# Performance work log

Measured on AMD Instinct MI355X. Metric: run time of the kernel, lower is better.

The kernel has to match this reference:

```python
import jax, jax.numpy as jnp
import numpy as np

N_NODES = 5000
N_EDGES = 80000
IN_DIM = 128
HID_DIM = 128
OUT_DIM = 64
NUM_HEADS = 1
BATCH = 8
NEG_SLOPE = 0.2  # DGL GATConv default leaky_relu negative_slope


def setup_inputs() -> dict:
    key = jax.random.key(0)
    ks = jax.random.split(key, 12)
    x = jax.random.normal(ks[0], (BATCH, N_NODES, IN_DIM), dtype=jnp.float32)
    src = jax.random.randint(ks[1], (N_EDGES,), 0, N_NODES)
    dst = jax.random.randint(ks[2], (N_EDGES,), 0, N_NODES)
    # layer1 params (fc has no bias in DGL GATConv; output bias present by default)
    s1 = 1.0 / np.sqrt(IN_DIM)
    W1 = jax.random.normal(ks[3], (IN_DIM, NUM_HEADS * HID_DIM), dtype=jnp.float32) * s1
    al1 = jax.random.normal(ks[4], (NUM_HEADS, HID_DIM), dtype=jnp.float32) * 0.1
    ar1 = jax.random.normal(ks[5], (NUM_HEADS, HID_DIM), dtype=jnp.float32) * 0.1
    b1 = jnp.zeros((NUM_HEADS * HID_DIM,), dtype=jnp.float32)
    # layer2 params
    s2 = 1.0 / np.sqrt(NUM_HEADS * HID_DIM)
    W2 = jax.random.normal(ks[6], (NUM_HEADS * HID_DIM, NUM_HEADS * OUT_DIM), dtype=jnp.float32) * s2
    al2 = jax.random.normal(ks[7], (NUM_HEADS, OUT_DIM), dtype=jnp.float32) * 0.1
    ar2 = jax.random.normal(ks[8], (NUM_HEADS, OUT_DIM), dtype=jnp.float32) * 0.1
    b2 = jnp.zeros((NUM_HEADS * OUT_DIM,), dtype=jnp.float32)
    return {"x": x, "W1": W1, "al1": al1, "ar1": ar1, "b1": b1,
            "W2": W2, "al2": al2, "ar2": ar2, "b2": b2,
            "src": src, "dst": dst}


def gat_layer(x, W, al, ar, b, src, dst, n_nodes):
    """DGL GATConv. x:[B,N,Din] W:[Din,H*F] al/ar:[H,F] b:[H*F] -> [B,N,H,F]."""
    B = x.shape[0]
    H, F = al.shape
    z = (x @ W).reshape(B, n_nodes, H, F)                 # [B,N,H,F]
    el = jnp.einsum('bnhf,hf->bnh', z, al)                # src-side attn term
    er = jnp.einsum('bnhf,hf->bnh', z, ar)                # dst-side attn term
    e = jax.nn.leaky_relu(el[:, src] + er[:, dst], NEG_SLOPE)  # [B,E,H]
    e = jnp.moveaxis(e, 1, 0)                             # [E,B,H]  edge-major for segment ops
    emax = jax.ops.segment_max(e, dst, num_segments=n_nodes)   # [N,B,H]
    ex = jnp.exp(e - emax[dst])
    denom = jax.ops.segment_sum(ex, dst, num_segments=n_nodes)  # [N,B,H]
    alpha = ex / denom[dst]                               # edge softmax over incoming edges
    zs = jnp.moveaxis(z[:, src], 1, 0)                    # [E,B,H,F] gathered source feats
    out = jax.ops.segment_sum(alpha[..., None] * zs, dst, num_segments=n_nodes)  # [N,B,H,F]
    return jnp.moveaxis(out, 0, 1) + b.reshape(1, 1, H, F)


def reference(x, W1, al1, ar1, b1, W2, al2, ar2, b2, src, dst):
    n_nodes = x.shape[1]
    h = gat_layer(x, W1, al1, ar1, b1, src, dst, n_nodes)  # [B,N,H,hid]
    B, N, H, Fh = h.shape
    h = h.reshape(B, N, H * Fh)                            # concat heads (H=1)
    o = gat_layer(h, W2, al2, ar2, b2, src, dst, n_nodes)  # [B,N,H,out]
    o = o.reshape(B * N, -1)                               # squeeze: [B*N, out]
    return jax.nn.softmax(o, axis=-1)
```

## Files before the change

kernel.cpp:

```cpp
#include <hip/hip_runtime.h>
#include <hip/hip_bf16.h>

#define N_NODES 5000
#define N_EDGES 80000
#define HID_DIM 128
#define OUT_DIM 64
#define BATCH 8
#define M_ROWS 40000
#define NEG_SLOPE 0.2f
#define BUCKET 96


typedef unsigned short ushort_t;
typedef unsigned int uint_t;
typedef __attribute__((ext_vector_type(8))) short short8;
typedef __attribute__((ext_vector_type(4))) float f32x4;

__device__ __forceinline__ float bf16_to_f32(ushort_t u) {
  return __uint_as_float(((uint_t)u) << 16);
}
__device__ __forceinline__ ushort_t f32_to_bf16(float f) {
  uint_t u = __float_as_uint(f);
  return (ushort_t)((u + 0x7FFF + ((u >> 16) & 1)) >> 16);
}

struct __attribute__((aligned(8))) us4 { ushort_t x, y, z, w; };

__global__ __launch_bounds__(256) void zero_pack_kernel(const float* __restrict__ W1,
                                                        const float* __restrict__ W2,
                                                        int* __restrict__ cnt,
                                                        ushort_t* __restrict__ Bp1,
                                                        ushort_t* __restrict__ Bp2) {
  int bid = blockIdx.x;
  if (bid < 20) {
    int i = bid * 256 + threadIdx.x;
    if (i < N_NODES) cnt[i] = 0;
    return;
  }
  int gid = (bid - 20) * 256 + threadIdx.x;
  if (gid >= 3072) return;
  const float* W; ushort_t* Bp; int NC, idx;
  if (gid < 2048) { W = W1; Bp = Bp1; NC = 128; idx = gid; }
  else            { W = W2; Bp = Bp2; NC = 64;  idx = gid - 2048; }
  int l = idx & 63, tt = idx >> 6;
  int T = NC / 16;
  int kc = tt / T, t = tt % T;
  int col = t * 16 + (l & 15);
  int krow = kc * 32 + (l >> 4) * 8;
  short8 vv;
#pragma unroll
  for (int j = 0; j < 8; j++) vv[j] = (short)f32_to_bf16(W[(size_t)(krow + j) * NC + col]);
  *(short8*)(Bp + (size_t)idx * 8) = vv;
}

template <int NC, bool A_F32, bool C_BF16, bool SCATTER>
__global__ __launch_bounds__(256) void gemm_mfma(const void* __restrict__ A,
                                                 const ushort_t* __restrict__ Bp,
                                                 void* __restrict__ C,
                                                 const float* __restrict__ al,
                                                 const float* __restrict__ ar,
                                                 float* __restrict__ el,
                                                 float* __restrict__ er,
                                                 const int* __restrict__ e_src,
                                                 const int* __restrict__ e_dst,
                                                 int* __restrict__ cnt,
                                                 int* __restrict__ srcs) {
  if (SCATTER) {
    int tid = threadIdx.x;
    if (tid < 128) {
      int i = blockIdx.x * 128 + tid;
      int d = e_dst[i];
      int pos = atomicAdd(&cnt[d], 1);
      if (pos < BUCKET) srcs[d * BUCKET + pos] = e_src[i];
    }
  }
  constexpr int T = NC / 16;
  int wave = threadIdx.x >> 6, lane = threadIdx.x & 63;
  int q = lane >> 4, m = lane & 15;
  int r0 = blockIdx.x * 64 + wave * 16;
  f32x4 acc[T];
#pragma unroll
  for (int t = 0; t < T; t++)
#pragma unroll
    for (int i = 0; i < 4; i++) acc[t][i] = 0.f;

  const short8* Bp8 = (const short8*)Bp;
  size_t arow = (size_t)(r0 + m) * 128;
#pragma unroll
  for (int kc = 0; kc < 4; kc++) {
    short8 af;
    if (A_F32) {
      const float* Ap = (const float*)A + arow + kc * 32 + q * 8;
      float4 v0 = *(const float4*)Ap;
      float4 v1 = *(const float4*)(Ap + 4);
      af[0] = (short)f32_to_bf16(v0.x); af[1] = (short)f32_to_bf16(v0.y);
      af[2] = (short)f32_to_bf16(v0.z); af[3] = (short)f32_to_bf16(v0.w);
      af[4] = (short)f32_to_bf16(v1.x); af[5] = (short)f32_to_bf16(v1.y);
      af[6] = (short)f32_to_bf16(v1.z); af[7] = (short)f32_to_bf16(v1.w);
    } else {
      const ushort_t* Ap = (const ushort_t*)A + arow + kc * 32 + q * 8;
      us4 a0 = *(const us4*)Ap;
      us4 a1 = *(const us4*)(Ap + 4);
      af[0] = (short)a0.x; af[1] = (short)a0.y; af[2] = (short)a0.z; af[3] = (short)a0.w;
      af[4] = (short)a1.x; af[5] = (short)a1.y; af[6] = (short)a1.z; af[7] = (short)a1.w;
    }
#pragma unroll
    for (int t = 0; t < T; t++) {
      short8 bf = Bp8[(kc * T + t) * 64 + lane];
      acc[t] = __builtin_amdgcn_mfma_f32_16x16x32_bf16(af, bf, acc[t], 0, 0, 0);
    }
  }
  float sl[4] = {0.f, 0.f, 0.f, 0.f}, sr[4] = {0.f, 0.f, 0.f, 0.f};
#pragma unroll
  for (int t = 0; t < T; t++) {
    float alv = al[t * 16 + m];
    float arv = ar[t * 16 + m];
#pragma unroll
    for (int i = 0; i < 4; i++) { sl[i] += acc[t][i] * alv; sr[i] += acc[t][i] * arv; }
  }
#pragma unroll
  for (int o = 1; o < 16; o <<= 1) {
#pragma unroll
    for (int i = 0; i < 4; i++) {
      sl[i] += __shfl_xor(sl[i], o, 64);
      sr[i] += __shfl_xor(sr[i], o, 64);
    }
  }
  if (m == 0) {
#pragma unroll
    for (int i = 0; i < 4; i++) {
      el[r0 + q * 4 + i] = sl[i];
      er[r0 + q * 4 + i] = sr[i];
    }
  }
#pragma unroll
  for (int t = 0; t < T; t++)
#pragma unroll
    for (int i = 0; i < 4; i++) {
      size_t off = (size_t)(r0 + q * 4 + i) * NC + t * 16 + m;
      if (C_BF16) ((ushort_t*)C)[off] = f32_to_bf16(acc[t][i]);
      else        ((float*)C)[off] = acc[t][i];
    }
}

template <int F, bool FINAL>
__global__ __launch_bounds__(256) void agg_kernel(const void* __restrict__ z,
                                                  const float* __restrict__ el,
                                                  const float* __restrict__ er,
                                                  const float* __restrict__ bias,
                                                  const int* __restrict__ cnt,
                                                  const int* __restrict__ srcs,
                                                  void* __restrict__ outp) {
  int id = (threadIdx.x >> 6) * gridDim.x + blockIdx.x;
  int lane = threadIdx.x & 63;
  int g = lane >> 4, l16 = lane & 15;
  int b = id & 7, n = id >> 3;
  int deg = cnt[n]; if (deg > BUCKET) deg = BUCKET;
  int off0 = n * BUCKET;
  int rbase = b * N_NODES;
  float er_n = er[rbase + n];

  constexpr int J = (F == 128) ? 8 : 4;
  float acc[J];
#pragma unroll
  for (int j = 0; j < J; j++) acc[j] = 0.f;
  float lsum = 0.f;

  for (int c = 0; c < deg; c += 64) {
    int j = c + lane;
    int s_my = 0;
    float w_my = 0.f;
    if (j < deg) {
      s_my = srcs[off0 + j];
      float e = el[rbase + s_my] + er_n;
      e = e > 0.f ? e : NEG_SLOPE * e;
      w_my = __expf(e);
      lsum += w_my;
    }
    int cl = deg - c; if (cl > 64) cl = 64;
    for (int k0 = 0; k0 < cl; k0 += 16) {
      float wk[4]; int sk[4];
#pragma unroll
      for (int u = 0; u < 4; u++) {
        int e_idx = k0 + u * 4 + g;
        wk[u] = __shfl(w_my, e_idx, 64);
        sk[u] = __shfl(s_my, e_idx, 64);
      }
      if (F == 128) {
        uint4 zw[4];
#pragma unroll
        for (int u = 0; u < 4; u++)
          zw[u] = *(const uint4*)((const ushort_t*)z + (size_t)(rbase + sk[u]) * F + l16 * 8);
#pragma unroll
        for (int u = 0; u < 4; u++) {
          acc[0] += wk[u] * bf16_to_f32((ushort_t)(zw[u].x & 0xFFFF));
          acc[1] += wk[u] * bf16_to_f32((ushort_t)(zw[u].x >> 16));
          acc[2] += wk[u] * bf16_to_f32((ushort_t)(zw[u].y & 0xFFFF));
          acc[3] += wk[u] * bf16_to_f32((ushort_t)(zw[u].y >> 16));
          acc[4] += wk[u] * bf16_to_f32((ushort_t)(zw[u].z & 0xFFFF));
          acc[5] += wk[u] * bf16_to_f32((ushort_t)(zw[u].z >> 16));
          acc[6] += wk[u] * bf16_to_f32((ushort_t)(zw[u].w & 0xFFFF));
          acc[7] += wk[u] * bf16_to_f32((ushort_t)(zw[u].w >> 16));
        }
      } else {
        uint2 zw[4];
#pragma unroll
        for (int u = 0; u < 4; u++)
          zw[u] = *(const uint2*)((const ushort_t*)z + (size_t)(rbase + sk[u]) * F + l16 * 4);
#pragma unroll
        for (int u = 0; u < 4; u++) {
          acc[0] += wk[u] * bf16_to_f32((ushort_t)(zw[u].x & 0xFFFF));
          acc[1] += wk[u] * bf16_to_f32((ushort_t)(zw[u].x >> 16));
          acc[2] += wk[u] * bf16_to_f32((ushort_t)(zw[u].y & 0xFFFF));
          acc[3] += wk[u] * bf16_to_f32((ushort_t)(zw[u].y >> 16));
        }
      }
    }
  }
#pragma unroll
  for (int j = 0; j < J; j++) {
    acc[j] += __shfl_xor(acc[j], 16, 64);
    acc[j] += __shfl_xor(acc[j], 32, 64);
  }
  float sum = lsum;
#pragma unroll
  for (int o = 32; o; o >>= 1) sum += __shfl_xor(sum, o, 64);
  float inv = (deg > 0) ? 1.f / sum : 0.f;

  if (!FINAL) {
    if (g == 0) {
      uint_t pk[4];
#pragma unroll
      for (int p = 0; p < 4; p++) {
        float o0 = acc[2 * p] * inv + bias[l16 * 8 + 2 * p];
        float o1 = acc[2 * p + 1] * inv + bias[l16 * 8 + 2 * p + 1];
        pk[p] = (uint_t)f32_to_bf16(o0) | ((uint_t)f32_to_bf16(o1) << 16);
      }
      *(uint4*)((ushort_t*)outp + (size_t)(rbase + n) * F + l16 * 8) =
          make_uint4(pk[0], pk[1], pk[2], pk[3]);
    }
  } else {
    float o[4];
#pragma unroll
    for (int j = 0; j < 4; j++) o[j] = acc[j] * inv + bias[l16 * 4 + j];
    float mm = fmaxf(fmaxf(o[0], o[1]), fmaxf(o[2], o[3]));
#pragma unroll
    for (int d = 1; d < 16; d <<= 1) mm = fmaxf(mm, __shfl_xor(mm, d, 64));
    float p0 = __expf(o[0] - mm), p1 = __expf(o[1] - mm);
    float p2 = __expf(o[2] - mm), p3 = __expf(o[3] - mm);
    float ss = p0 + p1 + p2 + p3;
#pragma unroll
    for (int d = 1; d < 16; d <<= 1) ss += __shfl_xor(ss, d, 64);
    if (g == 0) {
      float issv = 1.f / ss;
      *(float4*)((float*)outp + (size_t)(rbase + n) * F + l16 * 4) =
          make_float4(p0 * issv, p1 * issv, p2 * issv, p3 * issv);
    }
  }
}

extern "C" void kernel_launch(void* const* d_in, const int* in_sizes, int n_in,
                              void* d_out, int out_size, void* d_ws, size_t ws_size,
                              hipStream_t stream) {
  const float* x   = (const float*)d_in[0];
  const float* W1  = (const float*)d_in[1];
  const float* al1 = (const float*)d_in[2];
  const float* ar1 = (const float*)d_in[3];
  const float* b1  = (const float*)d_in[4];
  const float* W2  = (const float*)d_in[5];
  const float* al2 = (const float*)d_in[6];
  const float* ar2 = (const float*)d_in[7];
  const float* b2  = (const float*)d_in[8];
  const int* src = (const int*)d_in[9];
  const int* dst = (const int*)d_in[10];

  char* base = (char*)d_ws;
  ushort_t* Bp1 = (ushort_t*)base;
  ushort_t* Bp2 = Bp1 + 16384;
  ushort_t* z1  = (ushort_t*)(base + 49152);
  ushort_t* z2  = (ushort_t*)(base + 49152);
  ushort_t* h   = (ushort_t*)(base + 10289152);
  float* el1    = (float*)(base + 20529152);
  float* er1    = el1 + M_ROWS;
  float* el2    = er1 + M_ROWS;
  float* er2    = el2 + M_ROWS;
  int* cnt      = (int*)(base + 20529152 + 640000);
  int* srcs     = cnt + N_NODES;

  zero_pack_kernel<<<32, 256, 0, stream>>>(W1, W2, cnt, Bp1, Bp2);

  gemm_mfma<HID_DIM, true, true, true><<<M_ROWS / 64, 256, 0, stream>>>(
      x, Bp1, z1, al1, ar1, el1, er1, src, dst, cnt, srcs);

  agg_kernel<HID_DIM, false><<<M_ROWS / 4, 256, 0, stream>>>(z1, el1, er1, b1, cnt, srcs, h);

  gemm_mfma<OUT_DIM, false, true, false><<<M_ROWS / 64, 256, 0, stream>>>(
      h, Bp2, z2, al2, ar2, el2, er2, nullptr, nullptr, nullptr, nullptr);

  agg_kernel<OUT_DIM, true><<<M_ROWS / 4, 256, 0, stream>>>(z2, el2, er2, b2, cnt, srcs, d_out);
}
```

Measured before the change: 150.0 us.

## Reassociate layer-2 projection before layer-1 aggregation and fuse both GEMMs

Uses linearity of the attention-weighted sum to apply W2 to z1 before the layer-1 aggregation, so the mid aggregation gathers 64-wide rows instead of 128-wide ones. The layer-2 attention logits are derived as weighted sums of per-node projections plus a bias constant precomputed from b1·W2. Both GEMMs are fused into one kernel with a swizzled LDS staging tile, which removes a launch and the round trip of the 128-wide intermediate through global memory. This trades some extra rounding (projection done before the softmax-weighted sum, bf16 intermediates) for less gather traffic.

```diff
diff --git a/kernel.cpp b/kernel.cpp
--- a/kernel.cpp
+++ b/kernel.cpp
@@ -26,15 +26,52 @@
 
 struct __attribute__((aligned(8))) us4 { ushort_t x, y, z, w; };
 
+#define OFF_BP1   0u
+#define OFF_BP2   32768u
+#define OFF_CMETA 49152u
+#define OFF_CB    49184u
+#define OFF_Y     65536u
+#define OFF_EY    5185536u
+#define OFF_W     5505536u
+#define OFF_EL1   10625536u
+#define OFF_ER1   10785536u
+#define OFF_EL2   10945536u
+#define OFF_ER2   11105536u
+#define OFF_CNT   11265536u
+#define OFF_SRCS  11285536u
+
 __global__ __launch_bounds__(256) void zero_pack_kernel(const float* __restrict__ W1,
                                                         const float* __restrict__ W2,
+                                                        const float* __restrict__ b1,
+                                                        const float* __restrict__ b2,
+                                                        const float* __restrict__ al2,
+                                                        const float* __restrict__ ar2,
                                                         int* __restrict__ cnt,
                                                         ushort_t* __restrict__ Bp1,
-                                                        ushort_t* __restrict__ Bp2) {
+                                                        ushort_t* __restrict__ Bp2,
+                                                        float* __restrict__ cmeta,
+                                                        float* __restrict__ cb) {
   int bid = blockIdx.x;
   if (bid < 20) {
     int i = bid * 256 + threadIdx.x;
     if (i < N_NODES) cnt[i] = 0;
+    return;
+  }
+  if (bid == 32) {
+    int f = threadIdx.x;
+    if (f < 64) {
+      float c = 0.f;
+#pragma unroll 8
+      for (int k = 0; k < 128; k++) c += b1[k] * W2[(size_t)k * 64 + f];
+      cb[f] = c + b2[f];
+      float cl = c * al2[f], cr = c * ar2[f];
+#pragma unroll
+      for (int o = 32; o; o >>= 1) {
+        cl += __shfl_xor(cl, o, 64);
+        cr += __shfl_xor(cr, o, 64);
+      }
+      if (f == 0) { cmeta[0] = cl; cmeta[1] = cr; }
+    }
     return;
   }
   int gid = (bid - 20) * 256 + threadIdx.x;
@@ -53,19 +90,22 @@
   *(short8*)(Bp + (size_t)idx * 8) = vv;
 }
 
-template <int NC, bool A_F32, bool C_BF16, bool SCATTER>
-__global__ __launch_bounds__(256) void gemm_mfma(const void* __restrict__ A,
-                                                 const ushort_t* __restrict__ Bp,
-                                                 void* __restrict__ C,
-                                                 const float* __restrict__ al,
-                                                 const float* __restrict__ ar,
-                                                 float* __restrict__ el,
-                                                 float* __restrict__ er,
-                                                 const int* __restrict__ e_src,
-                                                 const int* __restrict__ e_dst,
-                                                 int* __restrict__ cnt,
-                                                 int* __restrict__ srcs) {
-  if (SCATTER) {
+__global__ __launch_bounds__(256) void gemm_fused(const float* __restrict__ A,
+                                                  const ushort_t* __restrict__ Bp1,
+                                                  const ushort_t* __restrict__ Bp2,
+                                                  const float* __restrict__ al1,
+                                                  const float* __restrict__ ar1,
+                                                  const float* __restrict__ al2,
+                                                  const float* __restrict__ ar2,
+                                                  float* __restrict__ el1,
+                                                  float* __restrict__ er1,
+                                                  ushort_t* __restrict__ y,
+                                                  float2* __restrict__ ey,
+                                                  const int* __restrict__ e_src,
+                                                  const int* __restrict__ e_dst,
+                                                  int* __restrict__ cnt,
+                                                  int* __restrict__ srcs) {
+  {
     int tid = threadIdx.x;
     if (tid < 128) {
       int i = blockIdx.x * 128 + tid;
@@ -74,83 +114,115 @@
       if (pos < BUCKET) srcs[d * BUCKET + pos] = e_src[i];
     }
   }
-  constexpr int T = NC / 16;
+  __shared__ ushort_t lds[64 * 128];
   int wave = threadIdx.x >> 6, lane = threadIdx.x & 63;
   int q = lane >> 4, m = lane & 15;
   int r0 = blockIdx.x * 64 + wave * 16;
-  f32x4 acc[T];
-#pragma unroll
-  for (int t = 0; t < T; t++)
+
+  f32x4 acc[8];
+#pragma unroll
+  for (int t = 0; t < 8; t++)
 #pragma unroll
     for (int i = 0; i < 4; i++) acc[t][i] = 0.f;
-
-  const short8* Bp8 = (const short8*)Bp;
+  const short8* B1 = (const short8*)Bp1;
   size_t arow = (size_t)(r0 + m) * 128;
 #pragma unroll
   for (int kc = 0; kc < 4; kc++) {
+    const float* Ap = A + arow + kc * 32 + q * 8;
+    float4 v0 = *(const float4*)Ap;
+    float4 v1 = *(const float4*)(Ap + 4);
     short8 af;
-    if (A_F32) {
-      const float* Ap = (const float*)A + arow + kc * 32 + q * 8;
-      float4 v0 = *(const float4*)Ap;
-      float4 v1 = *(const float4*)(Ap + 4);
-      af[0] = (short)f32_to_bf16(v0.x); af[1] = (short)f32_to_bf16(v0.y);
-      af[2] = (short)f32_to_bf16(v0.z); af[3] = (short)f32_to_bf16(v0.w);
-      af[4] = (short)f32_to_bf16(v1.x); af[5] = (short)f32_to_bf16(v1.y);
-      af[6] = (short)f32_to_bf16(v1.z); af[7] = (short)f32_to_bf16(v1.w);
-    } else {
-      const ushort_t* Ap = (const ushort_t*)A + arow + kc * 32 + q * 8;
-      us4 a0 = *(const us4*)Ap;
-      us4 a1 = *(const us4*)(Ap + 4);
-      af[0] = (short)a0.x; af[1] = (short)a0.y; af[2] = (short)a0.z; af[3] = (short)a0.w;
-      af[4] = (short)a1.x; af[5] = (short)a1.y; af[6] = (short)a1.z; af[7] = (short)a1.w;
-    }
-#pragma unroll
-    for (int t = 0; t < T; t++) {
-      short8 bf = Bp8[(kc * T + t) * 64 + lane];
-      acc[t] = __builtin_amdgcn_mfma_f32_16x16x32_bf16(af, bf, acc[t], 0, 0, 0);
-    }
-  }
-  float sl[4] = {0.f, 0.f, 0.f, 0.f}, sr[4] = {0.f, 0.f, 0.f, 0.f};
-#pragma unroll
-  for (int t = 0; t < T; t++) {
-    float alv = al[t * 16 + m];
-    float arv = ar[t * 16 + m];
-#pragma unroll
-    for (int i = 0; i < 4; i++) { sl[i] += acc[t][i] * alv; sr[i] += acc[t][i] * arv; }
-  }
-#pragma unroll
-  for (int o = 1; o < 16; o <<= 1) {
+    af[0] = (short)f32_to_bf16(v0.x); af[1] = (short)f32_to_bf16(v0.y);
+    af[2] = (short)f32_to_bf16(v0.z); af[3] = (short)f32_to_bf16(v0.w);
+    af[4] = (short)f32_to_bf16(v1.x); af[5] = (short)f32_to_bf16(v1.y);
+    af[6] = (short)f32_to_bf16(v1.z); af[7] = (short)f32_to_bf16(v1.w);
+#pragma unroll
+    for (int t = 0; t < 8; t++)
+      acc[t] = __builtin_amdgcn_mfma_f32_16x16x32_bf16(af, B1[(kc * 8 + t) * 64 + lane], acc[t], 0, 0, 0);
+  }
+  {
+    float sl[4] = {0.f, 0.f, 0.f, 0.f}, sr[4] = {0.f, 0.f, 0.f, 0.f};
+#pragma unroll
+    for (int t = 0; t < 8; t++) {
+      float alv = al1[t * 16 + m], arv = ar1[t * 16 + m];
+#pragma unroll
+      for (int i = 0; i < 4; i++) { sl[i] += acc[t][i] * alv; sr[i] += acc[t][i] * arv; }
+    }
+#pragma unroll
+    for (int o = 1; o < 16; o <<= 1)
+#pragma unroll
+      for (int i = 0; i < 4; i++) {
+        sl[i] += __shfl_xor(sl[i], o, 64);
+        sr[i] += __shfl_xor(sr[i], o, 64);
+      }
+    if (m == 0)
+#pragma unroll
+      for (int i = 0; i < 4; i++) {
+        el1[r0 + q * 4 + i] = sl[i];
+        er1[r0 + q * 4 + i] = sr[i];
+      }
+  }
+#pragma unroll
+  for (int t = 0; t < 8; t++)
 #pragma unroll
     for (int i = 0; i < 4; i++) {
-      sl[i] += __shfl_xor(sl[i], o, 64);
-      sr[i] += __shfl_xor(sr[i], o, 64);
-    }
-  }
-  if (m == 0) {
-#pragma unroll
-    for (int i = 0; i < 4; i++) {
-      el[r0 + q * 4 + i] = sl[i];
-      er[r0 + q * 4 + i] = sr[i];
-    }
-  }
-#pragma unroll
-  for (int t = 0; t < T; t++)
-#pragma unroll
-    for (int i = 0; i < 4; i++) {
-      size_t off = (size_t)(r0 + q * 4 + i) * NC + t * 16 + m;
-      if (C_BF16) ((ushort_t*)C)[off] = f32_to_bf16(acc[t][i]);
-      else        ((float*)C)[off] = acc[t][i];
-    }
-}
-
-template <int F, bool FINAL>
-__global__ __launch_bounds__(256) void agg_kernel(const void* __restrict__ z,
-                                                  const float* __restrict__ el,
-                                                  const float* __restrict__ er,
-                                                  const float* __restrict__ bias,
-                                                  const int* __restrict__ cnt,
-                                                  const int* __restrict__ srcs,
-                                                  void* __restrict__ outp) {
+      int row = q * 4 + i + wave * 16;
+      int byte = row * 256 + (t * 16 + m) * 2;
+      lds[(byte ^ ((row & 7) << 4)) >> 1] = f32_to_bf16(acc[t][i]);
+    }
+  __syncthreads();
+
+  f32x4 acc2[4];
+#pragma unroll
+  for (int t = 0; t < 4; t++)
+#pragma unroll
+    for (int i = 0; i < 4; i++) acc2[t][i] = 0.f;
+  const short8* B2 = (const short8*)Bp2;
+  int row2 = wave * 16 + m;
+#pragma unroll
+  for (int kc = 0; kc < 4; kc++) {
+    int byte = row2 * 256 + kc * 64 + q * 16;
+    short8 af2 = *(const short8*)((const char*)lds + (byte ^ ((row2 & 7) << 4)));
+#pragma unroll
+    for (int t = 0; t < 4; t++)
+      acc2[t] = __builtin_amdgcn_mfma_f32_16x16x32_bf16(af2, B2[(kc * 4 + t) * 64 + lane], acc2[t], 0, 0, 0);
+  }
+  {
+    float sl[4] = {0.f, 0.f, 0.f, 0.f}, sr[4] = {0.f, 0.f, 0.f, 0.f};
+#pragma unroll
+    for (int t = 0; t < 4; t++) {
+      float alv = al2[t * 16 + m], arv = ar2[t * 16 + m];
+#pragma unroll
+      for (int i = 0; i < 4; i++) { sl[i] += acc2[t][i] * alv; sr[i] += acc2[t][i] * arv; }
+    }
+#pragma unroll
+    for (int o = 1; o < 16; o <<= 1)
+#pragma unroll
+      for (int i = 0; i < 4; i++) {
+        sl[i] += __shfl_xor(sl[i], o, 64);
+        sr[i] += __shfl_xor(sr[i], o, 64);
+      }
+    if (m == 0)
+#pragma unroll
+      for (int i = 0; i < 4; i++) ey[r0 + q * 4 + i] = make_float2(sl[i], sr[i]);
+  }
+#pragma unroll
+  for (int t = 0; t < 4; t++)
+#pragma unroll
+    for (int i = 0; i < 4; i++)
+      y[(size_t)(r0 + q * 4 + i) * 64 + t * 16 + m] = f32_to_bf16(acc2[t][i]);
+}
+
+__global__ __launch_bounds__(256) void agg_mid(const ushort_t* __restrict__ y,
+                                               const float2* __restrict__ ey,
+                                               const float* __restrict__ el,
+                                               const float* __restrict__ er,
+                                               const int* __restrict__ cnt,
+                                               const int* __restrict__ srcs,
+                                               const float* __restrict__ cmeta,
+                                               ushort_t* __restrict__ w,
+                                               float* __restrict__ el2,
+                                               float* __restrict__ er2) {
   int id = (threadIdx.x >> 6) * gridDim.x + blockIdx.x;
   int lane = threadIdx.x & 63;
   int g = lane >> 4, l16 = lane & 15;
@@ -160,11 +232,8 @@
   int rbase = b * N_NODES;
   float er_n = er[rbase + n];
 
-  constexpr int J = (F == 128) ? 8 : 4;
-  float acc[J];
-#pragma unroll
-  for (int j = 0; j < J; j++) acc[j] = 0.f;
-  float lsum = 0.f;
+  float acc[4] = {0.f, 0.f, 0.f, 0.f};
+  float lsum = 0.f, sl2 = 0.f, sr2 = 0.f;
 
   for (int c = 0; c < deg; c += 64) {
     int j = c + lane;
@@ -176,6 +245,9 @@
       e = e > 0.f ? e : NEG_SLOPE * e;
       w_my = __expf(e);
       lsum += w_my;
+      float2 ev = ey[rbase + s_my];
+      sl2 += w_my * ev.x;
+      sr2 += w_my * ev.y;
     }
     int cl = deg - c; if (cl > 64) cl = 64;
     for (int k0 = 0; k0 < cl; k0 += 16) {
@@ -186,76 +258,121 @@
         wk[u] = __shfl(w_my, e_idx, 64);
         sk[u] = __shfl(s_my, e_idx, 64);
       }
-      if (F == 128) {
-        uint4 zw[4];
-#pragma unroll
-        for (int u = 0; u < 4; u++)
-          zw[u] = *(const uint4*)((const ushort_t*)z + (size_t)(rbase + sk[u]) * F + l16 * 8);
-#pragma unroll
-        for (int u = 0; u < 4; u++) {
-          acc[0] += wk[u] * bf16_to_f32((ushort_t)(zw[u].x & 0xFFFF));
-          acc[1] += wk[u] * bf16_to_f32((ushort_t)(zw[u].x >> 16));
-          acc[2] += wk[u] * bf16_to_f32((ushort_t)(zw[u].y & 0xFFFF));
-          acc[3] += wk[u] * bf16_to_f32((ushort_t)(zw[u].y >> 16));
-          acc[4] += wk[u] * bf16_to_f32((ushort_t)(zw[u].z & 0xFFFF));
-          acc[5] += wk[u] * bf16_to_f32((ushort_t)(zw[u].z >> 16));
-          acc[6] += wk[u] * bf16_to_f32((ushort_t)(zw[u].w & 0xFFFF));
-          acc[7] += wk[u] * bf16_to_f32((ushort_t)(zw[u].w >> 16));
-        }
-      } else {
-        uint2 zw[4];
-#pragma unroll
-        for (int u = 0; u < 4; u++)
-          zw[u] = *(const uint2*)((const ushort_t*)z + (size_t)(rbase + sk[u]) * F + l16 * 4);
-#pragma unroll
-        for (int u = 0; u < 4; u++) {
-          acc[0] += wk[u] * bf16_to_f32((ushort_t)(zw[u].x & 0xFFFF));
-          acc[1] += wk[u] * bf16_to_f32((ushort_t)(zw[u].x >> 16));
-          acc[2] += wk[u] * bf16_to_f32((ushort_t)(zw[u].y & 0xFFFF));
-          acc[3] += wk[u] * bf16_to_f32((ushort_t)(zw[u].y >> 16));
-        }
-      }
-    }
-  }
-#pragma unroll
-  for (int j = 0; j < J; j++) {
+      uint2 zw[4];
+#pragma unroll
+      for (int u = 0; u < 4; u++)
+        zw[u] = *(const uint2*)(y + (size_t)(rbase + sk[u]) * 64 + l16 * 4);
+#pragma unroll
+      for (int u = 0; u < 4; u++) {
+        acc[0] += wk[u] * bf16_to_f32((ushort_t)(zw[u].x & 0xFFFF));
+        acc[1] += wk[u] * bf16_to_f32((ushort_t)(zw[u].x >> 16));
+        acc[2] += wk[u] * bf16_to_f32((ushort_t)(zw[u].y & 0xFFFF));
+        acc[3] += wk[u] * bf16_to_f32((ushort_t)(zw[u].y >> 16));
+      }
+    }
+  }
+#pragma unroll
+  for (int j = 0; j < 4; j++) {
     acc[j] += __shfl_xor(acc[j], 16, 64);
     acc[j] += __shfl_xor(acc[j], 32, 64);
   }
   float sum = lsum;
 #pragma unroll
+  for (int o = 32; o; o >>= 1) {
+    sum += __shfl_xor(sum, o, 64);
+    sl2 += __shfl_xor(sl2, o, 64);
+    sr2 += __shfl_xor(sr2, o, 64);
+  }
+  float inv = (deg > 0) ? 1.f / sum : 0.f;
+
+  if (g == 0) {
+    uint_t pk0 = (uint_t)f32_to_bf16(acc[0] * inv) | ((uint_t)f32_to_bf16(acc[1] * inv) << 16);
+    uint_t pk1 = (uint_t)f32_to_bf16(acc[2] * inv) | ((uint_t)f32_to_bf16(acc[3] * inv) << 16);
+    *(uint2*)(w + (size_t)(rbase + n) * 64 + l16 * 4) = make_uint2(pk0, pk1);
+  }
+  if (lane == 0) {
+    el2[rbase + n] = sl2 * inv + cmeta[0];
+    er2[rbase + n] = sr2 * inv + cmeta[1];
+  }
+}
+
+__global__ __launch_bounds__(256) void agg_fin(const ushort_t* __restrict__ w,
+                                               const float* __restrict__ el,
+                                               const float* __restrict__ er,
+                                               const float* __restrict__ cb,
+                                               const int* __restrict__ cnt,
+                                               const int* __restrict__ srcs,
+                                               float* __restrict__ outp) {
+  int id = (threadIdx.x >> 6) * gridDim.x + blockIdx.x;
+  int lane = threadIdx.x & 63;
+  int g = lane >> 4, l16 = lane & 15;
+  int b = id & 7, n = id >> 3;
+  int deg = cnt[n]; if (deg > BUCKET) deg = BUCKET;
+  int off0 = n * BUCKET;
+  int rbase = b * N_NODES;
+  float er_n = er[rbase + n];
+
+  float acc[4] = {0.f, 0.f, 0.f, 0.f};
+  float lsum = 0.f;
+
+  for (int c = 0; c < deg; c += 64) {
+    int j = c + lane;
+    int s_my = 0;
+    float w_my = 0.f;
+    if (j < deg) {
+      s_my = srcs[off0 + j];
+      float e = el[rbase + s_my] + er_n;
+      e = e > 0.f ? e : NEG_SLOPE * e;
+      w_my = __expf(e);
+      lsum += w_my;
+    }
+    int cl = deg - c; if (cl > 64) cl = 64;
+    for (int k0 = 0; k0 < cl; k0 += 16) {
+      float wk[4]; int sk[4];
+#pragma unroll
+      for (int u = 0; u < 4; u++) {
+        int e_idx = k0 + u * 4 + g;
+        wk[u] = __shfl(w_my, e_idx, 64);
+        sk[u] = __shfl(s_my, e_idx, 64);
+      }
+      uint2 zw[4];
+#pragma unroll
+      for (int u = 0; u < 4; u++)
+        zw[u] = *(const uint2*)(w + (size_t)(rbase + sk[u]) * 64 + l16 * 4);
+#pragma unroll
+      for (int u = 0; u < 4; u++) {
+        acc[0] += wk[u] * bf16_to_f32((ushort_t)(zw[u].x & 0xFFFF));
+        acc[1] += wk[u] * bf16_to_f32((ushort_t)(zw[u].x >> 16));
+        acc[2] += wk[u] * bf16_to_f32((ushort_t)(zw[u].y & 0xFFFF));
+        acc[3] += wk[u] * bf16_to_f32((ushort_t)(zw[u].y >> 16));
+      }
+    }
+  }
+#pragma unroll
+  for (int j = 0; j < 4; j++) {
+    acc[j] += __shfl_xor(acc[j], 16, 64);
+    acc[j] += __shfl_xor(acc[j], 32, 64);
+  }
+  float sum = lsum;
+#pragma unroll
   for (int o = 32; o; o >>= 1) sum += __shfl_xor(sum, o, 64);
   float inv = (deg > 0) ? 1.f / sum : 0.f;
 
-  if (!FINAL) {
-    if (g == 0) {
-      uint_t pk[4];
-#pragma unroll
-      for (int p = 0; p < 4; p++) {
-        float o0 = acc[2 * p] * inv + bias[l16 * 8 + 2 * p];
-        float o1 = acc[2 * p + 1] * inv + bias[l16 * 8 + 2 * p + 1];
-        pk[p] = (uint_t)f32_to_bf16(o0) | ((uint_t)f32_to_bf16(o1) << 16);
-      }
-      *(uint4*)((ushort_t*)outp + (size_t)(rbase + n) * F + l16 * 8) =
-          make_uint4(pk[0], pk[1], pk[2], pk[3]);
-    }
-  } else {
-    float o[4];
-#pragma unroll
-    for (int j = 0; j < 4; j++) o[j] = acc[j] * inv + bias[l16 * 4 + j];
-    float mm = fmaxf(fmaxf(o[0], o[1]), fmaxf(o[2], o[3]));
-#pragma unroll
-    for (int d = 1; d < 16; d <<= 1) mm = fmaxf(mm, __shfl_xor(mm, d, 64));
-    float p0 = __expf(o[0] - mm), p1 = __expf(o[1] - mm);
-    float p2 = __expf(o[2] - mm), p3 = __expf(o[3] - mm);
-    float ss = p0 + p1 + p2 + p3;
-#pragma unroll
-    for (int d = 1; d < 16; d <<= 1) ss += __shfl_xor(ss, d, 64);
-    if (g == 0) {
-      float issv = 1.f / ss;
-      *(float4*)((float*)outp + (size_t)(rbase + n) * F + l16 * 4) =
-          make_float4(p0 * issv, p1 * issv, p2 * issv, p3 * issv);
-    }
+  float o[4];
+#pragma unroll
+  for (int j = 0; j < 4; j++) o[j] = acc[j] * inv + cb[l16 * 4 + j];
+  float mm = fmaxf(fmaxf(o[0], o[1]), fmaxf(o[2], o[3]));
+#pragma unroll
+  for (int d = 1; d < 16; d <<= 1) mm = fmaxf(mm, __shfl_xor(mm, d, 64));
+  float p0 = __expf(o[0] - mm), p1 = __expf(o[1] - mm);
+  float p2 = __expf(o[2] - mm), p3 = __expf(o[3] - mm);
+  float ss = p0 + p1 + p2 + p3;
+#pragma unroll
+  for (int d = 1; d < 16; d <<= 1) ss += __shfl_xor(ss, d, 64);
+  if (g == 0) {
+    float issv = 1.f / ss;
+    *(float4*)(outp + (size_t)(rbase + n) * 64 + l16 * 4) =
+        make_float4(p0 * issv, p1 * issv, p2 * issv, p3 * issv);
   }
 }
 
@@ -275,27 +392,26 @@
   const int* dst = (const int*)d_in[10];
 
   char* base = (char*)d_ws;
-  ushort_t* Bp1 = (ushort_t*)base;
-  ushort_t* Bp2 = Bp1 + 16384;
-  ushort_t* z1  = (ushort_t*)(base + 49152);
-  ushort_t* z2  = (ushort_t*)(base + 49152);
-  ushort_t* h   = (ushort_t*)(base + 10289152);
-  float* el1    = (float*)(base + 20529152);
-  float* er1    = el1 + M_ROWS;
-  float* el2    = er1 + M_ROWS;
-  float* er2    = el2 + M_ROWS;
-  int* cnt      = (int*)(base + 20529152 + 640000);
-  int* srcs     = cnt + N_NODES;
-
-  zero_pack_kernel<<<32, 256, 0, stream>>>(W1, W2, cnt, Bp1, Bp2);
-
-  gemm_mfma<HID_DIM, true, true, true><<<M_ROWS / 64, 256, 0, stream>>>(
-      x, Bp1, z1, al1, ar1, el1, er1, src, dst, cnt, srcs);
-
-  agg_kernel<HID_DIM, false><<<M_ROWS / 4, 256, 0, stream>>>(z1, el1, er1, b1, cnt, srcs, h);
-
-  gemm_mfma<OUT_DIM, false, true, false><<<M_ROWS / 64, 256, 0, stream>>>(
-      h, Bp2, z2, al2, ar2, el2, er2, nullptr, nullptr, nullptr, nullptr);
-
-  agg_kernel<OUT_DIM, true><<<M_ROWS / 4, 256, 0, stream>>>(z2, el2, er2, b2, cnt, srcs, d_out);
-}
+  ushort_t* Bp1  = (ushort_t*)(base + OFF_BP1);
+  ushort_t* Bp2  = (ushort_t*)(base + OFF_BP2);
+  float*    cmeta= (float*)(base + OFF_CMETA);
+  float*    cb   = (float*)(base + OFF_CB);
+  ushort_t* y    = (ushort_t*)(base + OFF_Y);
+  float2*   ey   = (float2*)(base + OFF_EY);
+  ushort_t* w    = (ushort_t*)(base + OFF_W);
+  float* el1 = (float*)(base + OFF_EL1);
+  float* er1 = (float*)(base + OFF_ER1);
+  float* el2 = (float*)(base + OFF_EL2);
+  float* er2 = (float*)(base + OFF_ER2);
+  int* cnt  = (int*)(base + OFF_CNT);
+  int* srcs = (int*)(base + OFF_SRCS);
+
+  zero_pack_kernel<<<33, 256, 0, stream>>>(W1, W2, b1, b2, al2, ar2, cnt, Bp1, Bp2, cmeta, cb);
+
+  gemm_fused<<<M_ROWS / 64, 256, 0, stream>>>(x, Bp1, Bp2, al1, ar1, al2, ar2,
+                                              el1, er1, y, ey, src, dst, cnt, srcs);
+
+  agg_mid<<<M_ROWS / 4, 256, 0, stream>>>(y, ey, el1, er1, cnt, srcs, cmeta, w, el2, er2);
+
+  agg_fin<<<M_ROWS / 4, 256, 0, stream>>>(w, el2, er2, cb, cnt, srcs, (float*)d_out);
+}
```

After: 143.3 us. 1.05x faster.
